# Kernel tuning notes

Measured on AMD Instinct MI355X. Metric: run time of the kernel, lower is better.

The kernel has to match this reference:

```python
import jax, jax.numpy as jnp
import numpy as np
import math

B, T, D, H = 2, 2048, 1024, 16
DH = D // H


def setup_inputs() -> dict:
    key = jax.random.key(0)
    k1, k2, k3 = jax.random.split(key, 3)
    scale_in = 1.0 / math.sqrt(D)
    x = jax.random.normal(k1, (B, T, D), dtype=jnp.float32)
    w_qkv = jax.random.normal(k2, (D, 3 * D), dtype=jnp.float32) * scale_in
    b_qkv = jnp.zeros((3 * D,), dtype=jnp.float32)
    w_out = jax.random.normal(k3, (D, D), dtype=jnp.float32) * scale_in
    b_out = jnp.zeros((D,), dtype=jnp.float32)
    return {"x": x, "w_qkv": w_qkv, "b_qkv": b_qkv, "w_out": w_out, "b_out": b_out}


def reference(x, w_qkv, b_qkv, w_out, b_out):
    # Fused QKV projection: [B,T,3D]
    qkv = x @ w_qkv + b_qkv
    q, k, v = jnp.split(qkv, 3, axis=-1)
    # [B,H,T,DH]
    q = q.reshape(B, T, H, DH).transpose(0, 2, 1, 3)
    k = k.reshape(B, T, H, DH).transpose(0, 2, 1, 3)
    v = v.reshape(B, T, H, DH).transpose(0, 2, 1, 3)
    # scores: [B,H,T,T]
    scores = jnp.einsum('bhqd,bhkd->bhqk', q, k) / math.sqrt(DH)
    causal_mask = jnp.tril(jnp.ones((T, T), dtype=bool))
    scores = jnp.where(causal_mask, scores, -1e10)
    attn = jax.nn.softmax(scores, axis=-1)
    out = jnp.einsum('bhqk,bhkd->bhqd', attn, v)
    out = out.transpose(0, 2, 1, 3).reshape(B, T, D)
    return out @ w_out + b_out
```

## Files before the change

kernel.cpp:

```cpp
#include <hip/hip_runtime.h>
#include <hip/hip_bf16.h>
#include <stdint.h>

#define Bsz  2
#define Tseq 2048
#define Dmod 1024
#define Hn   16
#define DHd  64

typedef short bf16x8 __attribute__((ext_vector_type(8)));
typedef float f32x4 __attribute__((ext_vector_type(4)));

__device__ __forceinline__ float bf2f(unsigned short u) {
  union { unsigned int i; float f; } v; v.i = ((unsigned int)u) << 16; return v.f;
}
__device__ __forceinline__ unsigned short f2bf(float f) {
  union { float f; unsigned int i; } v; v.f = f;
  unsigned int r = (v.i + 0x7fffu + ((v.i >> 16) & 1u)) >> 16;
  return (unsigned short)r;
}
__device__ __forceinline__ unsigned int pk_bf16(float a, float b) {
  union { __hip_bfloat162 h; unsigned int u; } u2;
  u2.h = __float22bfloat162_rn(make_float2(a, b));
  return u2.u;
}
__device__ __forceinline__ void gl_lds16(const unsigned short* g, unsigned short* l) {
  __builtin_amdgcn_global_load_lds(
      (const __attribute__((address_space(1))) void*)g,
      (__attribute__((address_space(3))) void*)l, 16, 0, 0);
}

#define QSCALE 0.1803368801f

__global__ __launch_bounds__(256) void prep(const float* __restrict__ x,
                                            const float* __restrict__ w_qkv,
                                            const float* __restrict__ w_out,
                                            unsigned short* __restrict__ xb,
                                            unsigned short* __restrict__ wqkvT,
                                            unsigned short* __restrict__ woutT) {
  __shared__ unsigned short tile[64][65];
  const int blk = blockIdx.x;
  if (blk < 2048) {
    int idx = blk * 2048 + threadIdx.x * 8;
    float4 a = *(const float4*)&x[idx];
    float4 b = *(const float4*)&x[idx + 4];
    unsigned short o[8];
    o[0] = f2bf(a.x); o[1] = f2bf(a.y); o[2] = f2bf(a.z); o[3] = f2bf(a.w);
    o[4] = f2bf(b.x); o[5] = f2bf(b.y); o[6] = f2bf(b.z); o[7] = f2bf(b.w);
    *(uint4*)&xb[idx] = *(const uint4*)o;
    return;
  }
  const float* in;
  unsigned short* out;
  int K = 1024, N, k0, n0;
  if (blk < 2048 + 768) {
    int t = blk - 2048;
    in = w_qkv; out = wqkvT; N = 3072;
    n0 = (t % 48) * 64; k0 = (t / 48) * 64;
  } else {
    int t = blk - 2816;
    in = w_out; out = woutT; N = 1024;
    n0 = (t % 16) * 64; k0 = (t / 16) * 64;
  }
  for (int i = threadIdx.x; i < 4096; i += 256) {
    int r = i >> 6, c = i & 63;
    tile[r][c] = f2bf(in[(size_t)(k0 + r) * N + n0 + c]);
  }
  __syncthreads();
  for (int i = threadIdx.x; i < 4096; i += 256) {
    int r = i >> 6, c = i & 63;
    out[(size_t)(n0 + r) * K + k0 + c] = tile[c][r];
  }
}

template<int MT, int NT>
__global__ __launch_bounds__(256) void gemm_bt(const unsigned short* __restrict__ A,
                                               const unsigned short* __restrict__ Bt,
                                               const float* __restrict__ bias,
                                               int M, int N, int K, int mode,
                                               float* __restrict__ outF,
                                               unsigned short* __restrict__ out0,
                                               unsigned short* __restrict__ out1,
                                               unsigned short* __restrict__ out2) {
  constexpr int IT = MT / 32;
  constexpr int JT = NT / 32;
  constexpr int AP = MT / 64;
  constexpr int BP = NT / 64;
  __shared__ unsigned short As[2][MT * 32];
  __shared__ unsigned short Bs[2][NT * 32];
  const int tid  = threadIdx.x;
  const int lane = tid & 63;
  const int w    = tid >> 6;
  const int m0   = blockIdx.x * MT;
  const int n0   = blockIdx.y * NT;
  const int wr   = (w >> 1) * (MT / 2);
  const int wc   = (w & 1) * (NT / 2);

  f32x4 acc[IT][JT];
  for (int i = 0; i < IT; i++)
    for (int j = 0; j < JT; j++)
      for (int v = 0; v < 4; v++) acc[i][j][v] = 0.0f;

  const int l16  = lane & 15;
  const int g    = lane >> 4;
  const int fkey = (l16 & 3) ^ ((l16 >> 2) & 3);

  const int csw = (((lane & 3) ^ ((lane >> 2) & 3) ^ ((lane >> 4) & 3)) & 3) * 8;
  const unsigned short* ga[AP];
  const unsigned short* gb[BP];
  unsigned short* la[2][AP];
  unsigned short* lb[2][BP];
#pragma unroll
  for (int p = 0; p < AP; p++) {
    int r = (MT / 4) * w + 16 * p + (lane >> 2);
    ga[p] = A + (size_t)(m0 + r) * K + csw;
    la[0][p] = &As[0][((MT / 4) * w + 16 * p) * 32];
    la[1][p] = &As[1][((MT / 4) * w + 16 * p) * 32];
  }
#pragma unroll
  for (int p = 0; p < BP; p++) {
    int r = (NT / 4) * w + 16 * p + (lane >> 2);
    gb[p] = Bt + (size_t)(n0 + r) * K + csw;
    lb[0][p] = &Bs[0][((NT / 4) * w + 16 * p) * 32];
    lb[1][p] = &Bs[1][((NT / 4) * w + 16 * p) * 32];
  }

#pragma unroll
  for (int p = 0; p < AP; p++) gl_lds16(ga[p], la[0][p]);
#pragma unroll
  for (int p = 0; p < BP; p++) gl_lds16(gb[p], lb[0][p]);
  __syncthreads();

  for (int kt = 0; kt < K; kt += 32) {
    const int cur = (kt >> 5) & 1, nxt = cur ^ 1;
    if (kt + 32 < K) {
#pragma unroll
      for (int p = 0; p < AP; p++) gl_lds16(ga[p] + kt + 32, la[nxt][p]);
#pragma unroll
      for (int p = 0; p < BP; p++) gl_lds16(gb[p] + kt + 32, lb[nxt][p]);
    }
    bf16x8 af[IT], bf[JT];
#pragma unroll
    for (int i = 0; i < IT; i++)
      af[i] = *(const bf16x8*)&As[cur][(wr + i * 16 + l16) * 32 + ((g ^ fkey) * 8)];
#pragma unroll
    for (int j = 0; j < JT; j++)
      bf[j] = *(const bf16x8*)&Bs[cur][(wc + j * 16 + l16) * 32 + ((g ^ fkey) * 8)];
#pragma unroll
    for (int i = 0; i < IT; i++)
#pragma unroll
      for (int j = 0; j < JT; j++)
        acc[i][j] = __builtin_amdgcn_mfma_f32_16x16x32_bf16(af[i], bf[j], acc[i][j], 0, 0, 0);
    __syncthreads();
  }

  const int q4 = g * 4;
#pragma unroll
  for (int i = 0; i < IT; i++)
#pragma unroll
    for (int j = 0; j < JT; j++) {
      const int mbase = m0 + wr + i * 16 + q4;
      const int n = n0 + wc + j * 16 + l16;
      float vals[4];
#pragma unroll
      for (int v = 0; v < 4; v++) vals[v] = acc[i][j][v] + bias[n];
      if (mode == 1) {
#pragma unroll
        for (int v = 0; v < 4; v++)
          outF[(size_t)(mbase + v) * N + n] = vals[v];
      } else {
        const int which = n >> 10;
        const int rem = n & 1023;
        const int h = rem >> 6, dd = rem & 63;
        const int b = mbase >> 11, t = mbase & 2047;
        if (which == 2) {
          uint2 uu;
          uu.x = pk_bf16(vals[0], vals[1]);
          uu.y = pk_bf16(vals[2], vals[3]);
          const int t2 = (t & ~63) | (t & 32) | (((t >> 2) & 3) << 3) | (((t >> 4) & 1) << 2);
          *(uint2*)&out2[((size_t)((b * Hn + h) * DHd + dd)) * Tseq + t2] = uu;
        } else if (which == 0) {
#pragma unroll
          for (int v = 0; v < 4; v++)
            out0[(size_t)((b * Hn + h) * Tseq + t + v) * DHd + dd] = f2bf(vals[v] * QSCALE);
        } else {
#pragma unroll
          for (int v = 0; v < 4; v++)
            out1[(size_t)((b * Hn + h) * Tseq + t + v) * DHd + dd] = f2bf(vals[v]);
        }
      }
    }
}

__global__ __launch_bounds__(256, 4) void attn_mfma(const unsigned short* __restrict__ Qb,
                                                    const unsigned short* __restrict__ Kb,
                                                    const unsigned short* __restrict__ Vtg,
                                                    unsigned short* __restrict__ O) {
  __shared__ unsigned short Ks[2][64 * 64];
  __shared__ unsigned short Vs[2][64 * 64];

  const int tid  = threadIdx.x;
  const int lane = tid & 63;
  const int w    = tid >> 6;
  const int g    = lane >> 4;
  const int l16  = lane & 15;
  const int bh   = blockIdx.x;
  const int tile = (int)gridDim.y - 1 - (int)blockIdx.y;
  const int q0w  = tile * 64 + w * 16;

  const unsigned short* Qp = Qb  + (size_t)bh * Tseq * DHd;
  const unsigned short* Kp = Kb  + (size_t)bh * Tseq * DHd;
  const unsigned short* Vp = Vtg + (size_t)bh * DHd * Tseq;

  bf16x8 qf[2];
#pragma unroll
  for (int ks = 0; ks < 2; ks++)
    qf[ks] = *(const bf16x8*)&Qp[(size_t)(q0w + l16) * DHd + ks * 32 + g * 8];

  f32x4 Oacc[4];
#pragma unroll
  for (int dt = 0; dt < 4; dt++)
#pragma unroll
    for (int v = 0; v < 4; v++) Oacc[dt][v] = 0.f;

  const f32x4 FZ = {0.f, 0.f, 0.f, 0.f};
  float lpart = 0.f;
  const int swz = l16 & 7;

  const int csw = (((lane & 7) ^ (lane >> 3)) & 7) * 8;
  const unsigned short* KgB = Kp + (size_t)(16 * w + (lane >> 3)) * DHd + csw;
  const unsigned short* VgB = Vp + (size_t)(16 * w + (lane >> 3)) * Tseq + csw;
  unsigned short* KsW[2] = { &Ks[0][16 * w * 64], &Ks[1][16 * w * 64] };
  unsigned short* VsW[2] = { &Vs[0][16 * w * 64], &Vs[1][16 * w * 64] };

  gl_lds16(KgB,             KsW[0]);
  gl_lds16(KgB + 8 * DHd,   KsW[0] + 8 * 64);
  gl_lds16(VgB,             VsW[0]);
  gl_lds16(VgB + 8 * Tseq,  VsW[0] + 8 * 64);
  __syncthreads();

  for (int c = 0; c <= tile; c++) {
    const int cur = c & 1, nxt = cur ^ 1;
    if (c < tile) {
      const size_t ko = (size_t)(c + 1) * 64 * DHd;
      const int    vo = (c + 1) * 64;
      gl_lds16(KgB + ko,            KsW[nxt]);
      gl_lds16(KgB + ko + 8 * DHd,  KsW[nxt] + 8 * 64);
      gl_lds16(VgB + vo,            VsW[nxt]);
      gl_lds16(VgB + vo + 8 * Tseq, VsW[nxt] + 8 * 64);
    }

    f32x4 st[4];
    {
      bf16x8 kf[4];
#pragma unroll
      for (int mt = 0; mt < 4; mt++)
        kf[mt] = *(const bf16x8*)&Ks[cur][(16 * mt + l16) * 64 + ((g ^ swz) * 8)];
#pragma unroll
      for (int mt = 0; mt < 4; mt++)
        st[mt] = __builtin_amdgcn_mfma_f32_16x16x32_bf16(kf[mt], qf[0], FZ, 0, 0, 0);
    }
    {
      bf16x8 kf[4];
#pragma unroll
      for (int mt = 0; mt < 4; mt++)
        kf[mt] = *(const bf16x8*)&Ks[cur][(16 * mt + l16) * 64 + (((4 + g) ^ swz) * 8)];
#pragma unroll
      for (int mt = 0; mt < 4; mt++)
        st[mt] = __builtin_amdgcn_mfma_f32_16x16x32_bf16(kf[mt], qf[1], st[mt], 0, 0, 0);
    }

    if (c == tile) {
      const int qg = q0w + l16;
#pragma unroll
      for (int mt = 0; mt < 4; mt++)
#pragma unroll
        for (int v = 0; v < 4; v++)
          if ((c * 64 + 16 * mt + 4 * g + v) > qg) st[mt][v] = -1e30f;
    }

    unsigned int pw[2][4];
#pragma unroll
    for (int mt = 0; mt < 4; mt++) {
      float p[4];
#pragma unroll
      for (int v = 0; v < 4; v++) { p[v] = __builtin_exp2f(st[mt][v]); lpart += p[v]; }
      pw[mt >> 1][(mt & 1) * 2 + 0] = pk_bf16(p[0], p[1]);
      pw[mt >> 1][(mt & 1) * 2 + 1] = pk_bf16(p[2], p[3]);
    }

#pragma unroll
    for (int ks = 0; ks < 2; ks++) {
      union { unsigned int u[4]; bf16x8 v8; } pu;
#pragma unroll
      for (int m = 0; m < 4; m++) pu.u[m] = pw[ks][m];
      const bf16x8 pf = pu.v8;
      bf16x8 vf[4];
#pragma unroll
      for (int dt = 0; dt < 4; dt++)
        vf[dt] = *(const bf16x8*)&Vs[cur][(16 * dt + l16) * 64 + (((4 * ks + g) ^ swz) * 8)];
#pragma unroll
      for (int dt = 0; dt < 4; dt++)
        Oacc[dt] = __builtin_amdgcn_mfma_f32_16x16x32_bf16(pf, vf[dt], Oacc[dt], 0, 0, 0);
    }

    __syncthreads();
  }

  float lrow = lpart;
  lrow += __shfl_xor(lrow, 16);
  lrow += __shfl_xor(lrow, 32);
  const float l0 = __shfl(lrow, 4 * g + 0);
  const float l1 = __shfl(lrow, 4 * g + 1);
  const float l2 = __shfl(lrow, 4 * g + 2);
  const float l3 = __shfl(lrow, 4 * g + 3);
  const float i0 = 1.f / l0, i1 = 1.f / l1, i2 = 1.f / l2, i3 = 1.f / l3;
  const int b = bh >> 4, h = bh & 15;
#pragma unroll
  for (int dt = 0; dt < 4; dt++) {
    const int d = h * DHd + 16 * dt + l16;
    const size_t r0 = (size_t)(b * Tseq + q0w + 4 * g) * Dmod + d;
    O[r0]            = f2bf(Oacc[dt][0] * i0);
    O[r0 + Dmod]     = f2bf(Oacc[dt][1] * i1);
    O[r0 + 2 * Dmod] = f2bf(Oacc[dt][2] * i2);
    O[r0 + 3 * Dmod] = f2bf(Oacc[dt][3] * i3);
  }
}

extern "C" void kernel_launch(void* const* d_in, const int* in_sizes, int n_in,
                              void* d_out, int out_size, void* d_ws, size_t ws_size,
                              hipStream_t stream) {
  (void)in_sizes; (void)n_in; (void)out_size; (void)ws_size;
  const float* x     = (const float*)d_in[0];
  const float* w_qkv = (const float*)d_in[1];
  const float* b_qkv = (const float*)d_in[2];
  const float* w_out = (const float*)d_in[3];
  const float* b_out = (const float*)d_in[4];
  float* out = (float*)d_out;

  unsigned short* ws    = (unsigned short*)d_ws;
  unsigned short* xb    = ws;
  unsigned short* wqkvT = xb    + (size_t)4194304;
  unsigned short* woutT = wqkvT + (size_t)3072 * 1024;
  unsigned short* Qb    = woutT + (size_t)1024 * 1024;
  unsigned short* Kb    = Qb + (size_t)4194304;
  unsigned short* Vt    = Kb + (size_t)4194304;
  unsigned short* Ob    = xb;

  prep<<<3072, 256, 0, stream>>>(x, w_qkv, w_out, xb, wqkvT, woutT);
  gemm_bt<128, 128><<<dim3(32, 24), 256, 0, stream>>>(xb, wqkvT, b_qkv, 4096, 3072, 1024, 0,
                                                      nullptr, Qb, Kb, Vt);
  attn_mfma<<<dim3(32, 32), 256, 0, stream>>>(Qb, Kb, Vt, Ob);
  gemm_bt<64, 64><<<dim3(64, 16), 256, 0, stream>>>(Ob, woutT, b_out, 4096, 1024, 1024, 1,
                                                    out, nullptr, nullptr, nullptr);
}
```

Measured before the change: 174.6 us.

## Switch attention to 32x32x16 MFMA with two waves per 64-query tile

Rewrites the causal attention kernel to use 32x32x16 bf16 MFMA instead of 16x16x32, so each wave owns 32 query rows. The block shrinks from 4 waves to 2, and each wave now loads more K/V rows into LDS. The V-transpose permutation in the QKV GEMM epilogue is changed to match the new fragment layout. This cuts the number of MFMA issues and LDS fragment reads per score tile, at the cost of more accumulator registers per wave and fewer waves per block to hide latency.

Result: slower. 191.2 us (+9.5%).

```diff
diff --git a/kernel.cpp b/kernel.cpp
--- a/kernel.cpp
+++ b/kernel.cpp
@@ -10,6 +10,7 @@
 
 typedef short bf16x8 __attribute__((ext_vector_type(8)));
 typedef float f32x4 __attribute__((ext_vector_type(4)));
+typedef float f32x16 __attribute__((ext_vector_type(16)));
 
 __device__ __forceinline__ float bf2f(unsigned short u) {
   union { unsigned int i; float f; } v; v.i = ((unsigned int)u) << 16; return v.f;
@@ -177,7 +178,7 @@
           uint2 uu;
           uu.x = pk_bf16(vals[0], vals[1]);
           uu.y = pk_bf16(vals[2], vals[3]);
-          const int t2 = (t & ~63) | (t & 32) | (((t >> 2) & 3) << 3) | (((t >> 4) & 1) << 2);
+          const int t2 = (t & ~12) | ((t & 4) << 1) | ((t & 8) >> 1);
           *(uint2*)&out2[((size_t)((b * Hn + h) * DHd + dd)) * Tseq + t2] = uu;
         } else if (which == 0) {
 #pragma unroll
@@ -192,7 +193,7 @@
     }
 }
 
-__global__ __launch_bounds__(256, 4) void attn_mfma(const unsigned short* __restrict__ Qb,
+__global__ __launch_bounds__(128, 3) void attn_mfma(const unsigned short* __restrict__ Qb,
                                                     const unsigned short* __restrict__ Kb,
                                                     const unsigned short* __restrict__ Vtg,
                                                     unsigned short* __restrict__ O) {
@@ -202,41 +203,45 @@
   const int tid  = threadIdx.x;
   const int lane = tid & 63;
   const int w    = tid >> 6;
-  const int g    = lane >> 4;
-  const int l16  = lane & 15;
+  const int l32  = lane & 31;
+  const int h    = lane >> 5;
   const int bh   = blockIdx.x;
   const int tile = (int)gridDim.y - 1 - (int)blockIdx.y;
-  const int q0w  = tile * 64 + w * 16;
+  const int q0w  = tile * 64 + w * 32;
 
   const unsigned short* Qp = Qb  + (size_t)bh * Tseq * DHd;
   const unsigned short* Kp = Kb  + (size_t)bh * Tseq * DHd;
   const unsigned short* Vp = Vtg + (size_t)bh * DHd * Tseq;
 
-  bf16x8 qf[2];
-#pragma unroll
-  for (int ks = 0; ks < 2; ks++)
-    qf[ks] = *(const bf16x8*)&Qp[(size_t)(q0w + l16) * DHd + ks * 32 + g * 8];
-
-  f32x4 Oacc[4];
-#pragma unroll
-  for (int dt = 0; dt < 4; dt++)
-#pragma unroll
-    for (int v = 0; v < 4; v++) Oacc[dt][v] = 0.f;
-
-  const f32x4 FZ = {0.f, 0.f, 0.f, 0.f};
+  bf16x8 qf[4];
+#pragma unroll
+  for (int t = 0; t < 4; t++)
+    qf[t] = *(const bf16x8*)&Qp[(size_t)(q0w + l32) * DHd + 16 * t + 8 * h];
+
+  f32x16 Oacc[2];
+#pragma unroll
+  for (int dt = 0; dt < 2; dt++)
+#pragma unroll
+    for (int v = 0; v < 16; v++) Oacc[dt][v] = 0.f;
+
+  f32x16 FZ16;
+#pragma unroll
+  for (int v = 0; v < 16; v++) FZ16[v] = 0.f;
+
   float lpart = 0.f;
-  const int swz = l16 & 7;
-
-  const int csw = (((lane & 7) ^ (lane >> 3)) & 7) * 8;
-  const unsigned short* KgB = Kp + (size_t)(16 * w + (lane >> 3)) * DHd + csw;
-  const unsigned short* VgB = Vp + (size_t)(16 * w + (lane >> 3)) * Tseq + csw;
-  unsigned short* KsW[2] = { &Ks[0][16 * w * 64], &Ks[1][16 * w * 64] };
-  unsigned short* VsW[2] = { &Vs[0][16 * w * 64], &Vs[1][16 * w * 64] };
-
-  gl_lds16(KgB,             KsW[0]);
-  gl_lds16(KgB + 8 * DHd,   KsW[0] + 8 * 64);
-  gl_lds16(VgB,             VsW[0]);
-  gl_lds16(VgB + 8 * Tseq,  VsW[0] + 8 * 64);
+  const int rsw = l32 & 7;
+
+  const int csw = (((lane & 7) ^ ((lane >> 3) & 7)) & 7) * 8;
+  const unsigned short* KgB = Kp + (size_t)(32 * w + (lane >> 3)) * DHd + csw;
+  const unsigned short* VgB = Vp + (size_t)(32 * w + (lane >> 3)) * Tseq + csw;
+  unsigned short* KsW[2] = { &Ks[0][32 * w * 64], &Ks[1][32 * w * 64] };
+  unsigned short* VsW[2] = { &Vs[0][32 * w * 64], &Vs[1][32 * w * 64] };
+
+#pragma unroll
+  for (int r = 0; r < 4; r++) {
+    gl_lds16(KgB + r * 8 * DHd,  KsW[0] + r * 512);
+    gl_lds16(VgB + r * 8 * Tseq, VsW[0] + r * 512);
+  }
   __syncthreads();
 
   for (int c = 0; c <= tile; c++) {
@@ -244,86 +249,72 @@
     if (c < tile) {
       const size_t ko = (size_t)(c + 1) * 64 * DHd;
       const int    vo = (c + 1) * 64;
-      gl_lds16(KgB + ko,            KsW[nxt]);
-      gl_lds16(KgB + ko + 8 * DHd,  KsW[nxt] + 8 * 64);
-      gl_lds16(VgB + vo,            VsW[nxt]);
-      gl_lds16(VgB + vo + 8 * Tseq, VsW[nxt] + 8 * 64);
-    }
-
-    f32x4 st[4];
-    {
-      bf16x8 kf[4];
-#pragma unroll
-      for (int mt = 0; mt < 4; mt++)
-        kf[mt] = *(const bf16x8*)&Ks[cur][(16 * mt + l16) * 64 + ((g ^ swz) * 8)];
-#pragma unroll
-      for (int mt = 0; mt < 4; mt++)
-        st[mt] = __builtin_amdgcn_mfma_f32_16x16x32_bf16(kf[mt], qf[0], FZ, 0, 0, 0);
-    }
-    {
-      bf16x8 kf[4];
-#pragma unroll
-      for (int mt = 0; mt < 4; mt++)
-        kf[mt] = *(const bf16x8*)&Ks[cur][(16 * mt + l16) * 64 + (((4 + g) ^ swz) * 8)];
-#pragma unroll
-      for (int mt = 0; mt < 4; mt++)
-        st[mt] = __builtin_amdgcn_mfma_f32_16x16x32_bf16(kf[mt], qf[1], st[mt], 0, 0, 0);
+#pragma unroll
+      for (int r = 0; r < 4; r++) {
+        gl_lds16(KgB + ko + r * 8 * DHd,  KsW[nxt] + r * 512);
+        gl_lds16(VgB + vo + r * 8 * Tseq, VsW[nxt] + r * 512);
+      }
+    }
+
+    f32x16 st2[2];
+#pragma unroll
+    for (int kt = 0; kt < 2; kt++) {
+      const int rowb = (32 * kt + l32) * 64;
+      bf16x8 kf0 = *(const bf16x8*)&Ks[cur][rowb + (((0 + h) ^ rsw) * 8)];
+      st2[kt] = __builtin_amdgcn_mfma_f32_32x32x16_bf16(kf0, qf[0], FZ16, 0, 0, 0);
+#pragma unroll
+      for (int t = 1; t < 4; t++) {
+        bf16x8 kf = *(const bf16x8*)&Ks[cur][rowb + (((2 * t + h) ^ rsw) * 8)];
+        st2[kt] = __builtin_amdgcn_mfma_f32_32x32x16_bf16(kf, qf[t], st2[kt], 0, 0, 0);
+      }
     }
 
     if (c == tile) {
-      const int qg = q0w + l16;
-#pragma unroll
-      for (int mt = 0; mt < 4; mt++)
-#pragma unroll
-        for (int v = 0; v < 4; v++)
-          if ((c * 64 + 16 * mt + 4 * g + v) > qg) st[mt][v] = -1e30f;
-    }
-
-    unsigned int pw[2][4];
-#pragma unroll
-    for (int mt = 0; mt < 4; mt++) {
-      float p[4];
-#pragma unroll
-      for (int v = 0; v < 4; v++) { p[v] = __builtin_exp2f(st[mt][v]); lpart += p[v]; }
-      pw[mt >> 1][(mt & 1) * 2 + 0] = pk_bf16(p[0], p[1]);
-      pw[mt >> 1][(mt & 1) * 2 + 1] = pk_bf16(p[2], p[3]);
-    }
-
-#pragma unroll
-    for (int ks = 0; ks < 2; ks++) {
+      const int qloc = 32 * w + l32;
+#pragma unroll
+      for (int kt = 0; kt < 2; kt++)
+#pragma unroll
+        for (int r = 0; r < 16; r++) {
+          const int kloc = 32 * kt + (r & 3) + 8 * (r >> 2) + 4 * h;
+          if (kloc > qloc) st2[kt][r] = -1e30f;
+        }
+    }
+
+    unsigned int pw[2][8];
+#pragma unroll
+    for (int kt = 0; kt < 2; kt++) {
+      float p[16];
+#pragma unroll
+      for (int r = 0; r < 16; r++) { p[r] = __builtin_exp2f(st2[kt][r]); lpart += p[r]; }
+#pragma unroll
+      for (int m = 0; m < 8; m++) pw[kt][m] = pk_bf16(p[2 * m], p[2 * m + 1]);
+    }
+
+#pragma unroll
+    for (int s = 0; s < 4; s++) {
       union { unsigned int u[4]; bf16x8 v8; } pu;
 #pragma unroll
-      for (int m = 0; m < 4; m++) pu.u[m] = pw[ks][m];
-      const bf16x8 pf = pu.v8;
-      bf16x8 vf[4];
-#pragma unroll
-      for (int dt = 0; dt < 4; dt++)
-        vf[dt] = *(const bf16x8*)&Vs[cur][(16 * dt + l16) * 64 + (((4 * ks + g) ^ swz) * 8)];
-#pragma unroll
-      for (int dt = 0; dt < 4; dt++)
-        Oacc[dt] = __builtin_amdgcn_mfma_f32_16x16x32_bf16(pf, vf[dt], Oacc[dt], 0, 0, 0);
+      for (int m = 0; m < 4; m++) pu.u[m] = pw[s >> 1][4 * (s & 1) + m];
+#pragma unroll
+      for (int dt = 0; dt < 2; dt++) {
+        bf16x8 vf = *(const bf16x8*)&Vs[cur][(32 * dt + l32) * 64 + (((2 * s + h) ^ rsw) * 8)];
+        Oacc[dt] = __builtin_amdgcn_mfma_f32_32x32x16_bf16(pu.v8, vf, Oacc[dt], 0, 0, 0);
+      }
     }
 
     __syncthreads();
   }
 
-  float lrow = lpart;
-  lrow += __shfl_xor(lrow, 16);
-  lrow += __shfl_xor(lrow, 32);
-  const float l0 = __shfl(lrow, 4 * g + 0);
-  const float l1 = __shfl(lrow, 4 * g + 1);
-  const float l2 = __shfl(lrow, 4 * g + 2);
-  const float l3 = __shfl(lrow, 4 * g + 3);
-  const float i0 = 1.f / l0, i1 = 1.f / l1, i2 = 1.f / l2, i3 = 1.f / l3;
-  const int b = bh >> 4, h = bh & 15;
-#pragma unroll
-  for (int dt = 0; dt < 4; dt++) {
-    const int d = h * DHd + 16 * dt + l16;
-    const size_t r0 = (size_t)(b * Tseq + q0w + 4 * g) * Dmod + d;
-    O[r0]            = f2bf(Oacc[dt][0] * i0);
-    O[r0 + Dmod]     = f2bf(Oacc[dt][1] * i1);
-    O[r0 + 2 * Dmod] = f2bf(Oacc[dt][2] * i2);
-    O[r0 + 3 * Dmod] = f2bf(Oacc[dt][3] * i3);
+  const float lrow = lpart + __shfl_xor(lpart, 32);
+  const float inv = 1.f / lrow;
+  const int b = bh >> 4, hh = bh & 15;
+#pragma unroll
+  for (int r = 0; r < 16; r++) {
+    const int qrow = (r & 3) + 8 * (r >> 2) + 4 * h;
+    const float il = __shfl(inv, qrow);
+    const size_t base = (size_t)(b * Tseq + q0w + qrow) * Dmod + hh * 64 + l32;
+    O[base]      = f2bf(Oacc[0][r] * il);
+    O[base + 32] = f2bf(Oacc[1][r] * il);
   }
 }
 
@@ -350,7 +341,7 @@
   prep<<<3072, 256, 0, stream>>>(x, w_qkv, w_out, xb, wqkvT, woutT);
   gemm_bt<128, 128><<<dim3(32, 24), 256, 0, stream>>>(xb, wqkvT, b_qkv, 4096, 3072, 1024, 0,
                                                       nullptr, Qb, Kb, Vt);
-  attn_mfma<<<dim3(32, 32), 256, 0, stream>>>(Qb, Kb, Vt, Ob);
+  attn_mfma<<<dim3(32, 32), 128, 0, stream>>>(Qb, Kb, Vt, Ob);
   gemm_bt<64, 64><<<dim3(64, 16), 256, 0, stream>>>(Ob, woutT, b_out, 4096, 1024, 1024, 1,
                                                     out, nullptr, nullptr, nullptr);
 }
```

## Remap GEMM and attention blocks across XCDs and vectorize weight transpose

Applied to the files above, without the earlier changes.

Block indices in the GEMM and attention kernels are remapped so that consecutively dispatched blocks, which land on different XCDs, cover contiguous chunks of the output and of the heads. The aim is for blocks sharing A/B tiles or K/V data to sit on the same XCD and reuse its L2. The weight convert-and-transpose kernel now uses float4 loads and 16-byte stores instead of scalar accesses. The attention remap also drops the old largest-causal-tile-first ordering, so dispatch now starts with small tiles, which may worsen tail balance.

Measured after the change: 187.5 us. 1.07x slower.

```diff
diff --git a/kernel.cpp b/kernel.cpp
--- a/kernel.cpp
+++ b/kernel.cpp
@@ -62,14 +62,21 @@
     in = w_out; out = woutT; N = 1024;
     n0 = (t % 16) * 64; k0 = (t / 16) * 64;
   }
-  for (int i = threadIdx.x; i < 4096; i += 256) {
+  for (int i = threadIdx.x * 4; i < 4096; i += 1024) {
     int r = i >> 6, c = i & 63;
-    tile[r][c] = f2bf(in[(size_t)(k0 + r) * N + n0 + c]);
+    float4 f = *(const float4*)&in[(size_t)(k0 + r) * N + n0 + c];
+    tile[r][c]     = f2bf(f.x);
+    tile[r][c + 1] = f2bf(f.y);
+    tile[r][c + 2] = f2bf(f.z);
+    tile[r][c + 3] = f2bf(f.w);
   }
   __syncthreads();
-  for (int i = threadIdx.x; i < 4096; i += 256) {
+  for (int i = threadIdx.x * 8; i < 4096; i += 2048) {
     int r = i >> 6, c = i & 63;
-    out[(size_t)(n0 + r) * K + k0 + c] = tile[c][r];
+    unsigned short o[8];
+#pragma unroll
+    for (int j = 0; j < 8; j++) o[j] = tile[c + j][r];
+    *(uint4*)&out[(size_t)(n0 + r) * K + k0 + c] = *(const uint4*)o;
   }
 }
 
@@ -91,8 +98,11 @@
   const int tid  = threadIdx.x;
   const int lane = tid & 63;
   const int w    = tid >> 6;
-  const int m0   = blockIdx.x * MT;
-  const int n0   = blockIdx.y * NT;
+  const int dlin = (int)blockIdx.x + (int)gridDim.x * (int)blockIdx.y;
+  const int qch  = ((int)gridDim.x * (int)gridDim.y) >> 3;
+  const int s    = (dlin & 7) * qch + (dlin >> 3);
+  const int m0   = (s % (int)gridDim.x) * MT;
+  const int n0   = (s / (int)gridDim.x) * NT;
   const int wr   = (w >> 1) * (MT / 2);
   const int wc   = (w & 1) * (NT / 2);
 
@@ -204,8 +214,10 @@
   const int w    = tid >> 6;
   const int g    = lane >> 4;
   const int l16  = lane & 15;
-  const int bh   = blockIdx.x;
-  const int tile = (int)gridDim.y - 1 - (int)blockIdx.y;
+  const int d    = (int)blockIdx.x + 32 * (int)blockIdx.y;
+  const int idx  = d >> 3;
+  const int bh   = 4 * (d & 7) + (idx & 3);
+  const int tile = idx >> 2;
   const int q0w  = tile * 64 + w * 16;
 
   const unsigned short* Qp = Qb  + (size_t)bh * Tseq * DHd;
@@ -318,8 +330,8 @@
   const int b = bh >> 4, h = bh & 15;
 #pragma unroll
   for (int dt = 0; dt < 4; dt++) {
-    const int d = h * DHd + 16 * dt + l16;
-    const size_t r0 = (size_t)(b * Tseq + q0w + 4 * g) * Dmod + d;
+    const int dcol = h * DHd + 16 * dt + l16;
+    const size_t r0 = (size_t)(b * Tseq + q0w + 4 * g) * Dmod + dcol;
     O[r0]            = f2bf(Oacc[dt][0] * i0);
     O[r0 + Dmod]     = f2bf(Oacc[dt][1] * i1);
     O[r0 + 2 * Dmod] = f2bf(Oacc[dt][2] * i2);
```
